# Optimization experiments

Measured on AMD Instinct MI355X. Metric: run time of the kernel, lower is better.

Reference implementation:

```python
import jax, jax.numpy as jnp
import numpy as np

BN_EPS = 1e-5


def conv1d(x, w, b, pad):
    # x: [N, Cin, L], w: [Cout, Cin, K], b: [Cout]
    out = jax.lax.conv_general_dilated(x, w, (1,), [(pad, pad)],
                                       dimension_numbers=("NCH", "OIH", "NCH"))
    return out + b[None, :, None]


def setup_inputs() -> dict:
    key = jax.random.key(0)
    ks = jax.random.split(key, 20)
    N, C, T, V = 64, 64, 256, 25
    S = 3                      # num_subset
    inter = C // 4             # inter_channels = out_channels // coff_embedding
    Cout = C
    ker_jpt = V if V % 2 else V - 1   # 25 -> spatial-attention kernel
    rr = 2

    x = jax.random.normal(ks[0], (N, C, T, V), dtype=jnp.float32)

    PA = 0.1 * jax.random.normal(ks[1], (S, V, V), dtype=jnp.float32)
    alpha = jnp.array([0.1], dtype=jnp.float32)
    Wa = 0.1 * jax.random.normal(ks[2], (S, inter, C), dtype=jnp.float32)
    ba = 0.01 * jax.random.normal(ks[3], (S, inter), dtype=jnp.float32)
    Wb = 0.1 * jax.random.normal(ks[4], (S, inter, C), dtype=jnp.float32)
    bb = 0.01 * jax.random.normal(ks[5], (S, inter), dtype=jnp.float32)
    Wd = 0.1 * jax.random.normal(ks[6], (S, Cout, C), dtype=jnp.float32)
    bd = 0.01 * jax.random.normal(ks[7], (S, Cout), dtype=jnp.float32)

    bn_gamma = 1.0 + 0.1 * jax.random.normal(ks[8], (Cout,), dtype=jnp.float32)
    bn_beta = 0.1 * jax.random.normal(ks[9], (Cout,), dtype=jnp.float32)

    Wsa = 0.05 * jax.random.normal(ks[10], (1, Cout, ker_jpt), dtype=jnp.float32)
    bsa = jnp.zeros((1,), dtype=jnp.float32)
    Wta = 0.05 * jax.random.normal(ks[11], (1, Cout, 9), dtype=jnp.float32)
    bta = jnp.zeros((1,), dtype=jnp.float32)

    W1 = 0.1 * jax.random.normal(ks[12], (Cout // rr, Cout), dtype=jnp.float32)
    b1 = jnp.zeros((Cout // rr,), dtype=jnp.float32)
    W2 = 0.1 * jax.random.normal(ks[13], (Cout, Cout // rr), dtype=jnp.float32)
    b2 = jnp.zeros((Cout,), dtype=jnp.float32)

    return dict(x=x, PA=PA, alpha=alpha, Wa=Wa, ba=ba, Wb=Wb, bb=bb, Wd=Wd, bd=bd,
                bn_gamma=bn_gamma, bn_beta=bn_beta, Wsa=Wsa, bsa=bsa, Wta=Wta,
                bta=bta, W1=W1, b1=b1, W2=W2, b2=b2)


def reference(x, PA, alpha, Wa, ba, Wb, bb, Wd, bd, bn_gamma, bn_beta,
              Wsa, bsa, Wta, bta, W1, b1, W2, b2):
    N, C, T, V = x.shape
    S, inter = Wa.shape[0], Wa.shape[1]
    denom = jnp.float32(inter * T)   # A1.size(-1) after view(N, V, inter*T)

    y = jnp.zeros((N, Wd.shape[1], T, V), dtype=x.dtype)
    for i in range(S):
        # 1x1 convs -> embeddings [N, inter, T, V]
        a = jnp.einsum("nctv,ic->nitv", x, Wa[i]) + ba[i][None, :, None, None]
        bf = jnp.einsum("nctv,ic->nitv", x, Wb[i]) + bb[i][None, :, None, None]
        # adaptive adjacency [N, V, V]
        A1 = jnp.tanh(jnp.einsum("nitv,nitw->nvw", a, bf) / denom)
        Ai = PA[i] + A1 * alpha[0]
        # graph aggregation + 1x1 conv_d
        z = jnp.einsum("nctv,nvw->nctw", x, Ai)
        y = y + jnp.einsum("nctv,oc->notv", z, Wd[i]) + bd[i][None, :, None, None]

    # eval-mode BatchNorm2d (running_mean=0, running_var=1)
    scale = bn_gamma / jnp.sqrt(1.0 + BN_EPS)
    y = y * scale[None, :, None, None] + bn_beta[None, :, None, None]
    # residual (in_channels == out_channels -> identity down)
    y = jax.nn.relu(y + x)

    # spatial SE gate: mean over T -> Conv1d over V
    se = y.mean(axis=2)                                   # [N, C, V]
    g = jax.nn.sigmoid(conv1d(se, Wsa, bsa, (Wsa.shape[-1] - 1) // 2))  # [N,1,V]
    y = y * g[:, :, None, :] + y

    # temporal SE gate: mean over V -> Conv1d over T
    se = y.mean(axis=3)                                   # [N, C, T]
    g = jax.nn.sigmoid(conv1d(se, Wta, bta, 4))           # [N, 1, T]
    y = y * g[:, :, :, None] + y

    # channel SE gate: global mean -> MLP
    se = y.mean(axis=(2, 3))                              # [N, C]
    h = jax.nn.relu(se @ W1.T + b1)
    g = jax.nn.sigmoid(h @ W2.T + b2)                     # [N, C]
    y = y * g[:, :, None, None] + y
    return y
```

## Files before the change

kernel.cpp:

```cpp
#include <hip/hip_runtime.h>
#include <math.h>


typedef __attribute__((ext_vector_type(8))) __bf16 bf16x8;
typedef __attribute__((ext_vector_type(4))) float  f32x4;

#define AIF_HALF 196608

__global__ __launch_bounds__(256, 3) void gcn_kA(const float* __restrict__ x,
                                                 const float* __restrict__ Wa,
                                                 const float* __restrict__ ba,
                                                 const float* __restrict__ Wb,
                                                 const float* __restrict__ bb,
                                                 float* __restrict__ Pws) {
    const int bid = blockIdx.x;
    const int n  = bid >> 4;
    const int tt = bid & 15;
    const int tid  = threadIdx.x;
    const int lane = tid & 63;
    const int wv   = tid >> 6;
    const int col  = lane & 15;
    const int quad = lane >> 4;

    __shared__ __align__(16) __bf16 xB[112 * 72];
    __shared__ __align__(16) __bf16 aT[3][32 * 72];
    __shared__ __align__(16) __bf16 bT[3][32 * 72];

    for (int j = tid; j < 12 * 72; j += 256) xB[100 * 72 + j] = (__bf16)0.f;
    for (int j = tid; j < 7 * 72; j += 256) {
        #pragma unroll
        for (int s = 0; s < 3; ++s) {
            aT[s][25 * 72 + j] = (__bf16)0.f;
            bT[s][25 * 72 + j] = (__bf16)0.f;
        }
    }

    bf16x8 waf0[3], waf1[3], wbf0[3], wbf1[3];
    float ba4[3][4], bb4[3][4];
    #pragma unroll
    for (int s = 0; s < 3; ++s) {
        const float* wap = Wa + (size_t)s * 1024 + col * 64 + quad * 8;
        const float* wbp = Wb + (size_t)s * 1024 + col * 64 + quad * 8;
        #pragma unroll
        for (int j = 0; j < 8; ++j) { waf0[s][j] = (__bf16)wap[j];      wbf0[s][j] = (__bf16)wbp[j]; }
        #pragma unroll
        for (int j = 0; j < 8; ++j) { waf1[s][j] = (__bf16)wap[32 + j]; wbf1[s][j] = (__bf16)wbp[32 + j]; }
        #pragma unroll
        for (int r = 0; r < 4; ++r) {
            ba4[s][r] = ba[s * 16 + quad * 4 + r];
            bb4[s][r] = bb[s * 16 + quad * 4 + r];
        }
    }

    f32x4 pacc[3];
    #pragma unroll
    for (int s = 0; s < 3; ++s) pacc[s] = (f32x4){0.f, 0.f, 0.f, 0.f};
    const int mi = wv >> 1, ni = wv & 1;

    const float* xbase = x + (size_t)n * 409600 + tt * 400;

    for (int cc = 0; cc < 4; ++cc) {
        __syncthreads();
        const float* xc = xbase + cc * 100;
        #pragma unroll
        for (int it = 0; it < 7; ++it) {
            int j4 = tid + it * 256;
            if (j4 < 1600) {
                int c  = j4 / 25;
                int qq = (j4 - c * 25) * 4;
                float4 xv = *(const float4*)(xc + c * 6400 + qq);
                __bf16* dst = &xB[qq * 72 + c];
                dst[0]   = (__bf16)xv.x;
                dst[72]  = (__bf16)xv.y;
                dst[144] = (__bf16)xv.z;
                dst[216] = (__bf16)xv.w;
            }
        }
        __syncthreads();

        #pragma unroll
        for (int s = 0; s < 3; ++s) {
            for (int jt = wv; jt < 7; jt += 4) {
                int q = jt * 16 + col;
                const __bf16* bp = &xB[q * 72 + quad * 8];
                bf16x8 b0 = *(const bf16x8*)bp;
                bf16x8 b1 = *(const bf16x8*)(bp + 32);
                f32x4 da = {0.f, 0.f, 0.f, 0.f}, db = {0.f, 0.f, 0.f, 0.f};
                da = __builtin_amdgcn_mfma_f32_16x16x32_bf16(waf0[s], b0, da, 0, 0, 0);
                da = __builtin_amdgcn_mfma_f32_16x16x32_bf16(waf1[s], b1, da, 0, 0, 0);
                db = __builtin_amdgcn_mfma_f32_16x16x32_bf16(wbf0[s], b0, db, 0, 0, 0);
                db = __builtin_amdgcn_mfma_f32_16x16x32_bf16(wbf1[s], b1, db, 0, 0, 0);
                if (q < 100) {
                    int tl = q / 25, v = q - tl * 25;
                    #pragma unroll
                    for (int r = 0; r < 4; ++r) {
                        int k = (quad * 4 + r) * 4 + tl;
                        aT[s][v * 72 + k] = (__bf16)(da[r] + ba4[s][r]);
                        bT[s][v * 72 + k] = (__bf16)(db[r] + bb4[s][r]);
                    }
                }
            }
        }
        __syncthreads();

        #pragma unroll
        for (int s = 0; s < 3; ++s) {
            #pragma unroll
            for (int k0 = 0; k0 < 64; k0 += 32) {
                bf16x8 af  = *(const bf16x8*)&aT[s][(mi * 16 + col) * 72 + k0 + quad * 8];
                bf16x8 bfr = *(const bf16x8*)&bT[s][(ni * 16 + col) * 72 + k0 + quad * 8];
                pacc[s] = __builtin_amdgcn_mfma_f32_16x16x32_bf16(af, bfr, pacc[s], 0, 0, 0);
            }
        }
    }

    #pragma unroll
    for (int s = 0; s < 3; ++s) {
        #pragma unroll
        for (int r = 0; r < 4; ++r) {
            int v = mi * 16 + quad * 4 + r;
            int w = ni * 16 + col;
            if (v < 25 && w < 25)
                atomicAdd(&Pws[(size_t)(s * 64 + n) * 625 + v * 25 + w], pacc[s][r]);
        }
    }
}

__global__ __launch_bounds__(256) void gcn_kB(const float* __restrict__ Pws,
                                              const float* __restrict__ PA,
                                              const float* __restrict__ alpha,
                                              __bf16* __restrict__ aiF) {
    int j = blockIdx.x * 256 + threadIdx.x;
    if (j < 120000) {
        int sn = j / 625;
        int r  = j - sn * 625;
        int s  = sn >> 6;
        float val = PA[s * 625 + r] + alpha[0] * tanhf(Pws[j] * (1.f / 4096.f));
        int k  = r / 25;
        int nn = r - k * 25;
        int vt = nn >> 4, colx = nn & 15;
        int idx = ((sn * 2 + vt) << 9) + (colx << 5) + k;
        __bf16 h = (__bf16)val;
        aiF[idx]            = h;
        aiF[AIF_HALF + idx] = (__bf16)(val - (float)h);
    }
}

__global__ __launch_bounds__(256, 3) void gcn_kC(const float* __restrict__ x,
                                              const __bf16* __restrict__ aiF,
                                              const float* __restrict__ Wd,
                                              const float* __restrict__ bd,
                                              const float* __restrict__ gamma,
                                              const float* __restrict__ beta,
                                              float* __restrict__ y1,
                                              float* __restrict__ meanT) {
    const int bid = blockIdx.x;
    const int tt = bid & 15;
    const int n  = bid >> 4;
    const int tid  = threadIdx.x;
    const int lane = tid & 63;
    const int wv   = tid >> 6;
    const int col  = lane & 15;
    const int quad = lane >> 4;

    __shared__ __align__(16) __bf16 xB[112 * 72];
    __shared__ __align__(16) __bf16 uL[256 * 40];

    for (int j = tid; j < 12 * 72; j += 256) xB[100 * 72 + j] = (__bf16)0.f;
    for (int j = tid; j < 256 * 15; j += 256) {
        int r = j / 15;
        int e = j - r * 15;
        uL[r * 40 + 25 + e] = (__bf16)0.f;
    }

    bf16x8 aiH[3][2], aiL[3][2];
    #pragma unroll
    for (int s = 0; s < 3; ++s) {
        #pragma unroll
        for (int vt = 0; vt < 2; ++vt) {
            const __bf16* p = aiF + ((size_t)((s * 64 + n) * 2 + vt)) * 512
                                  + col * 32 + quad * 8;
            aiH[s][vt] = *(const bf16x8*)p;
            aiL[s][vt] = *(const bf16x8*)(p + AIF_HALF);
        }
    }

    bf16x8 wd0[3], wd1[3];
    #pragma unroll
    for (int s = 0; s < 3; ++s) {
        const float* wdp = Wd + (size_t)(s * 64 + wv * 16 + col) * 64 + quad * 8;
        #pragma unroll
        for (int j = 0; j < 8; ++j) wd0[s][j] = (__bf16)wdp[j];
        #pragma unroll
        for (int j = 0; j < 8; ++j) wd1[s][j] = (__bf16)wdp[32 + j];
    }

    float scv[4], btv[4], bdsv[4];
    #pragma unroll
    for (int ml = 0; ml < 4; ++ml) {
        int o = (wv * 4 + ml) * 4 + quad;
        scv[ml]  = gamma[o] * rsqrtf(1.f + 1e-5f);
        btv[ml]  = beta[o];
        bdsv[ml] = bd[o] + bd[64 + o] + bd[128 + o];
    }

    float msum[4][2];
    #pragma unroll
    for (int ml = 0; ml < 4; ++ml) { msum[ml][0] = 0.f; msum[ml][1] = 0.f; }

    const float* xbase = x + (size_t)n * 409600 + tt * 400;

    for (int cc = 0; cc < 4; ++cc) {
        f32x4 acc[4][2];
        #pragma unroll
        for (int ml = 0; ml < 4; ++ml) {
            acc[ml][0] = (f32x4){0.f, 0.f, 0.f, 0.f};
            acc[ml][1] = (f32x4){0.f, 0.f, 0.f, 0.f};
        }

        __syncthreads();
        const float* xc = xbase + cc * 100;
        #pragma unroll
        for (int it = 0; it < 7; ++it) {
            int j4 = tid + it * 256;
            if (j4 < 1600) {
                int c  = j4 / 25;
                int qq = (j4 - c * 25) * 4;
                float4 xv = *(const float4*)(xc + c * 6400 + qq);
                __bf16* dst = &xB[qq * 72 + c];
                dst[0]   = (__bf16)xv.x;
                dst[72]  = (__bf16)xv.y;
                dst[144] = (__bf16)xv.z;
                dst[216] = (__bf16)xv.w;
            }
        }
        __syncthreads();

        #pragma unroll
        for (int s = 0; s < 3; ++s) {
            #pragma unroll
            for (int qt = 0; qt < 7; ++qt) {
                const __bf16* bp = &xB[(qt * 16 + col) * 72 + quad * 8];
                bf16x8 b0 = *(const bf16x8*)bp;
                bf16x8 b1 = *(const bf16x8*)(bp + 32);
                f32x4 u = {0.f, 0.f, 0.f, 0.f};
                u = __builtin_amdgcn_mfma_f32_16x16x32_bf16(wd0[s], b0, u, 0, 0, 0);
                u = __builtin_amdgcn_mfma_f32_16x16x32_bf16(wd1[s], b1, u, 0, 0, 0);
                int q = qt * 16 + col;
                if (q < 100) {
                    int trel = q / 25, v = q - trel * 25;
                    int rowbase = ((wv * 16 + quad * 4) * 4 + trel) * 40 + v;
                    uL[rowbase]       = (__bf16)u[0];
                    uL[rowbase + 160] = (__bf16)u[1];
                    uL[rowbase + 320] = (__bf16)u[2];
                    uL[rowbase + 480] = (__bf16)u[3];
                }
            }
            #pragma unroll
            for (int ml = 0; ml < 4; ++ml) {
                int row = (wv * 4 + ml) * 16 + col;
                bf16x8 af = *(const bf16x8*)&uL[row * 40 + quad * 8];
                acc[ml][0] = __builtin_amdgcn_mfma_f32_16x16x32_bf16(af, aiH[s][0], acc[ml][0], 0, 0, 0);
                acc[ml][1] = __builtin_amdgcn_mfma_f32_16x16x32_bf16(af, aiH[s][1], acc[ml][1], 0, 0, 0);
                acc[ml][0] = __builtin_amdgcn_mfma_f32_16x16x32_bf16(af, aiL[s][0], acc[ml][0], 0, 0, 0);
                acc[ml][1] = __builtin_amdgcn_mfma_f32_16x16x32_bf16(af, aiL[s][1], acc[ml][1], 0, 0, 0);
            }
        }

        #pragma unroll
        for (int ml = 0; ml < 4; ++ml) {
            int o = (wv * 4 + ml) * 4 + quad;
            #pragma unroll
            for (int vt = 0; vt < 2; ++vt) {
                int v = vt * 16 + col;
                if (v < 25) {
                    const size_t base =
                        ((size_t)(n * 64 + o) * 256 + tt * 16 + cc * 4) * 25 + v;
                    float ms = 0.f;
                    #pragma unroll
                    for (int r = 0; r < 4; ++r) {
                        float val = scv[ml] * (acc[ml][vt][r] + bdsv[ml]) + btv[ml]
                                  + x[base + r * 25];
                        val = val > 0.f ? val : 0.f;
                        y1[base + r * 25] = val;
                        ms += val;
                    }
                    msum[ml][vt] += ms;
                }
            }
        }
    }

    #pragma unroll
    for (int ml = 0; ml < 4; ++ml) {
        int o = (wv * 4 + ml) * 4 + quad;
        #pragma unroll
        for (int vt = 0; vt < 2; ++vt) {
            int v = vt * 16 + col;
            if (v < 25)
                atomicAdd(&meanT[(n * 64 + o) * 25 + v], msum[ml][vt]);
        }
    }
}

__global__ __launch_bounds__(256) void gcn_kD(const float* __restrict__ meanT,
                                              const float* __restrict__ Wsa,
                                              const float* __restrict__ bsa,
                                              float* __restrict__ g2p) {
    const int n = blockIdx.x;
    const int tid = threadIdx.x;
    __shared__ float sm[1600], wl[1600];
    for (int j = tid; j < 1600; j += 256) {
        sm[j] = meanT[n * 1600 + j] * (1.f / 256.f);
        wl[j] = Wsa[j];
    }
    __syncthreads();
    if (tid < 25) {
        float acc = bsa[0];
        for (int c = 0; c < 64; ++c) {
            #pragma unroll
            for (int k = 0; k < 25; ++k) {
                int j = tid + k - 12;
                if (j >= 0 && j < 25) acc += sm[c * 25 + j] * wl[c * 25 + k];
            }
        }
        g2p[n * 25 + tid] = 1.f + 1.f / (1.f + expf(-acc));
    }
}

__global__ __launch_bounds__(256) void gcn_kE(const float* __restrict__ y1,
                                              const float* __restrict__ g2p,
                                              float* __restrict__ M2) {
    const int bid = blockIdx.x;
    const int n = bid >> 6;
    const int tid = threadIdx.x;
    __shared__ float yl[6400];
    __shared__ float g2l[25];
    const float4* yp = (const float4*)(y1 + (size_t)bid * 6400);
    float4* ylv = (float4*)yl;
    for (int j = tid; j < 1600; j += 256) ylv[j] = yp[j];
    if (tid < 25) g2l[tid] = g2p[n * 25 + tid];
    __syncthreads();
    float sum = 0.f;
    #pragma unroll
    for (int v = 0; v < 25; ++v) sum += yl[tid * 25 + v] * g2l[v];
    M2[bid * 256 + tid] = sum * 0.04f;
}

__global__ __launch_bounds__(256) void gcn_kFG(const float* __restrict__ M2,
                                               const float* __restrict__ Wta,
                                               const float* __restrict__ bta,
                                               const float* __restrict__ W1,
                                               const float* __restrict__ b1,
                                               const float* __restrict__ W2,
                                               const float* __restrict__ b2,
                                               float* __restrict__ g3p,
                                               float* __restrict__ g4p) {
    const int n = blockIdx.x;
    const int tid = threadIdx.x;
    __shared__ float m2L[64 * 260];
    __shared__ float wl[576];
    __shared__ float g3l[256], part[256], M3[64], h[32];

    for (int j = tid; j < 16384; j += 256) {
        int c = j >> 8, t = j & 255;
        m2L[c * 260 + t] = M2[(size_t)n * 16384 + j];
    }
    for (int j = tid; j < 576; j += 256) wl[j] = Wta[j];
    __syncthreads();

    {
        const int t = tid;
        float acc = bta[0];
        for (int c = 0; c < 64; ++c) {
            const float* mp = &m2L[c * 260];
            #pragma unroll
            for (int k = 0; k < 9; ++k) {
                int j = t + k - 4;
                if (j >= 0 && j < 256) acc += mp[j] * wl[c * 9 + k];
            }
        }
        float g3 = 1.f + 1.f / (1.f + expf(-acc));
        g3l[t] = g3;
        g3p[n * 256 + t] = g3;
    }
    __syncthreads();

    {
        const int c = tid >> 2, q = tid & 3;
        float p = 0.f;
        const float* mp = &m2L[c * 260 + q * 64];
        #pragma unroll 16
        for (int j = 0; j < 64; ++j) p += mp[j] * g3l[q * 64 + j];
        part[tid] = p;
    }
    __syncthreads();
    if (tid < 64)
        M3[tid] = (part[tid * 4] + part[tid * 4 + 1] + part[tid * 4 + 2] +
                   part[tid * 4 + 3]) * (1.f / 256.f);
    __syncthreads();
    if (tid < 32) {
        float acc = b1[tid];
        #pragma unroll 16
        for (int cc = 0; cc < 64; ++cc) acc += W1[tid * 64 + cc] * M3[cc];
        h[tid] = acc > 0.f ? acc : 0.f;
    }
    __syncthreads();
    if (tid < 64) {
        float acc = b2[tid];
        #pragma unroll
        for (int j = 0; j < 32; ++j) acc += W2[tid * 32 + j] * h[j];
        g4p[n * 64 + tid] = 1.f + 1.f / (1.f + expf(-acc));
    }
}

__global__ __launch_bounds__(256) void gcn_kH(float* __restrict__ y,
                                              const float* __restrict__ g2p,
                                              const float* __restrict__ g3p,
                                              const float* __restrict__ g4p) {
    const int bid = blockIdx.x;
    const int n = bid >> 6;
    const int tid = threadIdx.x;
    __shared__ float g3l[256], g2l[25];
    g3l[tid] = g3p[n * 256 + tid];
    if (tid < 25) g2l[tid] = g2p[n * 25 + tid];
    const float g4 = g4p[bid];
    __syncthreads();
    float4* yp = (float4*)(y + (size_t)bid * 6400);
    for (int f = tid; f < 1600; f += 256) {
        float4 val = yp[f];
        float* vv = (float*)&val;
        const int base = f * 4;
        #pragma unroll
        for (int k = 0; k < 4; ++k) {
            int idx = base + k;
            int t = (int)(((unsigned long long)idx * 1374389535ull) >> 35);
            int v = idx - t * 25;
            vv[k] *= g2l[v] * g3l[t] * g4;
        }
        yp[f] = val;
    }
}

extern "C" void kernel_launch(void* const* d_in, const int* in_sizes, int n_in,
                              void* d_out, int out_size, void* d_ws, size_t ws_size,
                              hipStream_t stream) {
    const float* x     = (const float*)d_in[0];
    const float* PA    = (const float*)d_in[1];
    const float* alpha = (const float*)d_in[2];
    const float* Wa    = (const float*)d_in[3];
    const float* ba    = (const float*)d_in[4];
    const float* Wb    = (const float*)d_in[5];
    const float* bb    = (const float*)d_in[6];
    const float* Wd    = (const float*)d_in[7];
    const float* bd    = (const float*)d_in[8];
    const float* gamma = (const float*)d_in[9];
    const float* beta  = (const float*)d_in[10];
    const float* Wsa   = (const float*)d_in[11];
    const float* bsa   = (const float*)d_in[12];
    const float* Wta   = (const float*)d_in[13];
    const float* bta   = (const float*)d_in[14];
    const float* W1    = (const float*)d_in[15];
    const float* b1    = (const float*)d_in[16];
    const float* W2    = (const float*)d_in[17];
    const float* b2    = (const float*)d_in[18];

    float* out = (float*)d_out;
    float* ws  = (float*)d_ws;

    float*  Pws   = ws;
    float*  meanT = ws + 120000;
    __bf16* aiF   = (__bf16*)(ws + 222400);
    float*  M2    = ws + 419008;
    float*  g2p   = ws + 4613312;
    float*  g3p   = ws + 4614912;
    float*  g4p   = ws + 4631296;

    hipMemsetAsync(ws, 0, 222400 * sizeof(float), stream);
    hipMemsetAsync(aiF, 0, 786432, stream);

    gcn_kA<<<1024, 256, 0, stream>>>(x, Wa, ba, Wb, bb, Pws);
    gcn_kB<<<469, 256, 0, stream>>>(Pws, PA, alpha, aiF);
    gcn_kC<<<1024, 256, 0, stream>>>(x, aiF, Wd, bd, gamma, beta, out, meanT);
    gcn_kD<<<64, 256, 0, stream>>>(meanT, Wsa, bsa, g2p);
    gcn_kE<<<4096, 256, 0, stream>>>(out, g2p, M2);
    gcn_kFG<<<64, 256, 0, stream>>>(M2, Wta, bta, W1, b1, W2, b2, g3p, g4p);
    gcn_kH<<<4096, 256, 0, stream>>>(out, g2p, g3p, g4p);
}
```

Baseline: 593.9 us.

## Stage gcn_kC epilogue through per-wave LDS for coalesced float4 output stores

Each wave now owns 16 output channels end to end. It loads x as float4 once and keeps those values in registers for the residual, which removes the second scalar global read of x in the epilogue. The BN-scaled accumulators are first written to a per-wave LDS buffer (aliased with the uL scratch). They are then read back, combined with x, passed through ReLU, and written to y1 as coalesced float4 stores. Partial row sums are reduced through LDS atomics before the global atomicAdd. The cost is more LDS traffic, extra registers for the cached x vectors, and per-wave re-zeroing of the padding.

```diff
diff --git a/kernel.cpp b/kernel.cpp
--- a/kernel.cpp
+++ b/kernel.cpp
@@ -164,13 +164,16 @@
     const int quad = lane >> 4;
 
     __shared__ __align__(16) __bf16 xB[112 * 72];
-    __shared__ __align__(16) __bf16 uL[256 * 40];
+    __shared__ __align__(16) unsigned char uY[4 * 6656];
+
+    __bf16* uLw = (__bf16*)(uY + wv * 6656);
+    float*  ySw = (float*) (uY + wv * 6656);
 
     for (int j = tid; j < 12 * 72; j += 256) xB[100 * 72 + j] = (__bf16)0.f;
-    for (int j = tid; j < 256 * 15; j += 256) {
-        int r = j / 15;
-        int e = j - r * 15;
-        uL[r * 40 + 25 + e] = (__bf16)0.f;
+    {
+        __bf16* rz = uLw + lane * 40;
+        #pragma unroll
+        for (int k = 25; k < 32; ++k) rz[k] = (__bf16)0.f;
     }
 
     bf16x8 aiH[3][2], aiL[3][2];
@@ -198,17 +201,18 @@
     float scv[4], btv[4], bdsv[4];
     #pragma unroll
     for (int ml = 0; ml < 4; ++ml) {
-        int o = (wv * 4 + ml) * 4 + quad;
+        int o = wv * 16 + ml * 4 + quad;
         scv[ml]  = gamma[o] * rsqrtf(1.f + 1e-5f);
         btv[ml]  = beta[o];
         bdsv[ml] = bd[o] + bd[64 + o] + bd[128 + o];
     }
 
-    float msum[4][2];
-    #pragma unroll
-    for (int ml = 0; ml < 4; ++ml) { msum[ml][0] = 0.f; msum[ml][1] = 0.f; }
-
-    const float* xbase = x + (size_t)n * 409600 + tt * 400;
+    f32x4 msA[7];
+    #pragma unroll
+    for (int it = 0; it < 7; ++it) msA[it] = (f32x4){0.f, 0.f, 0.f, 0.f};
+
+    const float* xgw = x  + (size_t)(n * 64 + wv * 16) * 6400 + tt * 400;
+    float*       ygw = y1 + (size_t)(n * 64 + wv * 16) * 6400 + tt * 400;
 
     for (int cc = 0; cc < 4; ++cc) {
         f32x4 acc[4][2];
@@ -219,19 +223,21 @@
         }
 
         __syncthreads();
-        const float* xc = xbase + cc * 100;
+        const float* xc = xgw + cc * 100;
+        float4 xv[7];
         #pragma unroll
         for (int it = 0; it < 7; ++it) {
-            int j4 = tid + it * 256;
-            if (j4 < 1600) {
-                int c  = j4 / 25;
-                int qq = (j4 - c * 25) * 4;
-                float4 xv = *(const float4*)(xc + c * 6400 + qq);
+            int j = lane + it * 64;
+            if (j < 400) {
+                int cl = j / 25;
+                int qq = (j - cl * 25) * 4;
+                xv[it] = *(const float4*)(xc + cl * 6400 + qq);
+                int c = wv * 16 + cl;
                 __bf16* dst = &xB[qq * 72 + c];
-                dst[0]   = (__bf16)xv.x;
-                dst[72]  = (__bf16)xv.y;
-                dst[144] = (__bf16)xv.z;
-                dst[216] = (__bf16)xv.w;
+                dst[0]   = (__bf16)xv[it].x;
+                dst[72]  = (__bf16)xv[it].y;
+                dst[144] = (__bf16)xv[it].z;
+                dst[216] = (__bf16)xv[it].w;
             }
         }
         __syncthreads();
@@ -249,17 +255,16 @@
                 int q = qt * 16 + col;
                 if (q < 100) {
                     int trel = q / 25, v = q - trel * 25;
-                    int rowbase = ((wv * 16 + quad * 4) * 4 + trel) * 40 + v;
-                    uL[rowbase]       = (__bf16)u[0];
-                    uL[rowbase + 160] = (__bf16)u[1];
-                    uL[rowbase + 320] = (__bf16)u[2];
-                    uL[rowbase + 480] = (__bf16)u[3];
+                    int rowbase = (quad * 16 + trel) * 40 + v;
+                    uLw[rowbase]       = (__bf16)u[0];
+                    uLw[rowbase + 160] = (__bf16)u[1];
+                    uLw[rowbase + 320] = (__bf16)u[2];
+                    uLw[rowbase + 480] = (__bf16)u[3];
                 }
             }
             #pragma unroll
             for (int ml = 0; ml < 4; ++ml) {
-                int row = (wv * 4 + ml) * 16 + col;
-                bf16x8 af = *(const bf16x8*)&uL[row * 40 + quad * 8];
+                bf16x8 af = *(const bf16x8*)&uLw[(ml * 16 + col) * 40 + quad * 8];
                 acc[ml][0] = __builtin_amdgcn_mfma_f32_16x16x32_bf16(af, aiH[s][0], acc[ml][0], 0, 0, 0);
                 acc[ml][1] = __builtin_amdgcn_mfma_f32_16x16x32_bf16(af, aiH[s][1], acc[ml][1], 0, 0, 0);
                 acc[ml][0] = __builtin_amdgcn_mfma_f32_16x16x32_bf16(af, aiL[s][0], acc[ml][0], 0, 0, 0);
@@ -269,37 +274,67 @@
 
         #pragma unroll
         for (int ml = 0; ml < 4; ++ml) {
-            int o = (wv * 4 + ml) * 4 + quad;
+            int ol = ml * 4 + quad;
             #pragma unroll
             for (int vt = 0; vt < 2; ++vt) {
                 int v = vt * 16 + col;
                 if (v < 25) {
-                    const size_t base =
-                        ((size_t)(n * 64 + o) * 256 + tt * 16 + cc * 4) * 25 + v;
-                    float ms = 0.f;
                     #pragma unroll
-                    for (int r = 0; r < 4; ++r) {
-                        float val = scv[ml] * (acc[ml][vt][r] + bdsv[ml]) + btv[ml]
-                                  + x[base + r * 25];
-                        val = val > 0.f ? val : 0.f;
-                        y1[base + r * 25] = val;
-                        ms += val;
-                    }
-                    msum[ml][vt] += ms;
+                    for (int r = 0; r < 4; ++r)
+                        ySw[ol * 104 + r * 25 + v] =
+                            scv[ml] * (acc[ml][vt][r] + bdsv[ml]) + btv[ml];
                 }
             }
         }
-    }
-
-    #pragma unroll
-    for (int ml = 0; ml < 4; ++ml) {
-        int o = (wv * 4 + ml) * 4 + quad;
-        #pragma unroll
-        for (int vt = 0; vt < 2; ++vt) {
-            int v = vt * 16 + col;
-            if (v < 25)
-                atomicAdd(&meanT[(n * 64 + o) * 25 + v], msum[ml][vt]);
-        }
+
+        float* yc2 = ygw + cc * 100;
+        #pragma unroll
+        for (int it = 0; it < 7; ++it) {
+            int j = lane + it * 64;
+            if (j < 400) {
+                int cl = j / 25;
+                int qq = (j - cl * 25) * 4;
+                f32x4 yv = *(const f32x4*)&ySw[cl * 104 + qq];
+                float4 o4;
+                o4.x = yv[0] + xv[it].x; o4.x = o4.x > 0.f ? o4.x : 0.f;
+                o4.y = yv[1] + xv[it].y; o4.y = o4.y > 0.f ? o4.y : 0.f;
+                o4.z = yv[2] + xv[it].z; o4.z = o4.z > 0.f ? o4.z : 0.f;
+                o4.w = yv[3] + xv[it].w; o4.w = o4.w > 0.f ? o4.w : 0.f;
+                *(float4*)(yc2 + cl * 6400 + qq) = o4;
+                msA[it][0] += o4.x;
+                msA[it][1] += o4.y;
+                msA[it][2] += o4.z;
+                msA[it][3] += o4.w;
+            }
+        }
+
+        {
+            __bf16* rz = uLw + lane * 40;
+            #pragma unroll
+            for (int k = 25; k < 32; ++k) rz[k] = (__bf16)0.f;
+        }
+    }
+
+    __syncthreads();
+    float* msW = (float*)xB + wv * 1008;
+    for (int j2 = lane; j2 < 400; j2 += 64) msW[j2] = 0.f;
+    #pragma unroll
+    for (int it = 0; it < 7; ++it) {
+        int j = lane + it * 64;
+        if (j < 400) {
+            int cl = j / 25;
+            int qq = (j - cl * 25) * 4;
+            #pragma unroll
+            for (int k = 0; k < 4; ++k) {
+                int q = qq + k;
+                int v = q >= 75 ? q - 75 : (q >= 50 ? q - 50 : (q >= 25 ? q - 25 : q));
+                atomicAdd(&msW[cl * 25 + v], msA[it][k]);
+            }
+        }
+    }
+    for (int j2 = lane; j2 < 400; j2 += 64) {
+        int cl = j2 / 25, v = j2 - cl * 25;
+        atomicAdd(&meanT[(n * 64 + wv * 16 + cl) * 25 + v], msW[j2]);
     }
 }
 
```

After: 671.3 us. +13.0%, slower.

## Stage GCN output through per-wave LDS for coalesced stores and reuse staged residual

Applied to the files above, without the earlier changes.

gcn_kC's intermediate LDS buffer becomes a per-wave region that also serves as a float staging area for the output tile. Results are then written to y1 as coalesced float4 rows instead of scattered scalar stores. The residual is now read from the bf16 copy of x already in LDS rather than re-read from global memory. This cuts global traffic and uncoalesced stores, but the residual is rounded to bf16, and the padding columns must be re-zeroed every chunk because the staging area overlaps them.

```diff
diff --git a/kernel.cpp b/kernel.cpp
--- a/kernel.cpp
+++ b/kernel.cpp
@@ -164,13 +164,16 @@
     const int quad = lane >> 4;
 
     __shared__ __align__(16) __bf16 xB[112 * 72];
-    __shared__ __align__(16) __bf16 uL[256 * 40];
+    __shared__ __align__(16) unsigned char uY[4 * 6656];
+
+    __bf16* uLw = (__bf16*)(uY + wv * 6656);
+    float*  ySw = (float*) (uY + wv * 6656);
 
     for (int j = tid; j < 12 * 72; j += 256) xB[100 * 72 + j] = (__bf16)0.f;
-    for (int j = tid; j < 256 * 15; j += 256) {
-        int r = j / 15;
-        int e = j - r * 15;
-        uL[r * 40 + 25 + e] = (__bf16)0.f;
+    {
+        __bf16* rz = uLw + lane * 40;
+        #pragma unroll
+        for (int k = 25; k < 32; ++k) rz[k] = (__bf16)0.f;
     }
 
     bf16x8 aiH[3][2], aiL[3][2];
@@ -198,7 +201,7 @@
     float scv[4], btv[4], bdsv[4];
     #pragma unroll
     for (int ml = 0; ml < 4; ++ml) {
-        int o = (wv * 4 + ml) * 4 + quad;
+        int o = wv * 16 + ml * 4 + quad;
         scv[ml]  = gamma[o] * rsqrtf(1.f + 1e-5f);
         btv[ml]  = beta[o];
         bdsv[ml] = bd[o] + bd[64 + o] + bd[128 + o];
@@ -209,6 +212,7 @@
     for (int ml = 0; ml < 4; ++ml) { msum[ml][0] = 0.f; msum[ml][1] = 0.f; }
 
     const float* xbase = x + (size_t)n * 409600 + tt * 400;
+    float*       ygw   = y1 + (size_t)(n * 64 + wv * 16) * 6400 + tt * 400;
 
     for (int cc = 0; cc < 4; ++cc) {
         f32x4 acc[4][2];
@@ -249,17 +253,16 @@
                 int q = qt * 16 + col;
                 if (q < 100) {
                     int trel = q / 25, v = q - trel * 25;
-                    int rowbase = ((wv * 16 + quad * 4) * 4 + trel) * 40 + v;
-                    uL[rowbase]       = (__bf16)u[0];
-                    uL[rowbase + 160] = (__bf16)u[1];
-                    uL[rowbase + 320] = (__bf16)u[2];
-                    uL[rowbase + 480] = (__bf16)u[3];
+                    int rowbase = (quad * 16 + trel) * 40 + v;
+                    uLw[rowbase]       = (__bf16)u[0];
+                    uLw[rowbase + 160] = (__bf16)u[1];
+                    uLw[rowbase + 320] = (__bf16)u[2];
+                    uLw[rowbase + 480] = (__bf16)u[3];
                 }
             }
             #pragma unroll
             for (int ml = 0; ml < 4; ++ml) {
-                int row = (wv * 4 + ml) * 16 + col;
-                bf16x8 af = *(const bf16x8*)&uL[row * 40 + quad * 8];
+                bf16x8 af = *(const bf16x8*)&uLw[(ml * 16 + col) * 40 + quad * 8];
                 acc[ml][0] = __builtin_amdgcn_mfma_f32_16x16x32_bf16(af, aiH[s][0], acc[ml][0], 0, 0, 0);
                 acc[ml][1] = __builtin_amdgcn_mfma_f32_16x16x32_bf16(af, aiH[s][1], acc[ml][1], 0, 0, 0);
                 acc[ml][0] = __builtin_amdgcn_mfma_f32_16x16x32_bf16(af, aiL[s][0], acc[ml][0], 0, 0, 0);
@@ -269,31 +272,51 @@
 
         #pragma unroll
         for (int ml = 0; ml < 4; ++ml) {
-            int o = (wv * 4 + ml) * 4 + quad;
+            int ol = ml * 4 + quad;
+            int o  = wv * 16 + ol;
             #pragma unroll
             for (int vt = 0; vt < 2; ++vt) {
                 int v = vt * 16 + col;
                 if (v < 25) {
-                    const size_t base =
-                        ((size_t)(n * 64 + o) * 256 + tt * 16 + cc * 4) * 25 + v;
                     float ms = 0.f;
                     #pragma unroll
                     for (int r = 0; r < 4; ++r) {
+                        float resid = (float)xB[(r * 25 + v) * 72 + o];
                         float val = scv[ml] * (acc[ml][vt][r] + bdsv[ml]) + btv[ml]
-                                  + x[base + r * 25];
+                                  + resid;
                         val = val > 0.f ? val : 0.f;
-                        y1[base + r * 25] = val;
+                        ySw[ol * 104 + r * 25 + v] = val;
                         ms += val;
                     }
                     msum[ml][vt] += ms;
                 }
             }
         }
+
+        float* yc2 = ygw + cc * 100;
+        #pragma unroll
+        for (int it = 0; it < 7; ++it) {
+            int j = lane + it * 64;
+            if (j < 400) {
+                int cl = j / 25;
+                int qq = (j - cl * 25) * 4;
+                f32x4 yv = *(const f32x4*)&ySw[cl * 104 + qq];
+                float4 o4;
+                o4.x = yv[0]; o4.y = yv[1]; o4.z = yv[2]; o4.w = yv[3];
+                *(float4*)(yc2 + cl * 6400 + qq) = o4;
+            }
+        }
+
+        {
+            __bf16* rz = uLw + lane * 40;
+            #pragma unroll
+            for (int k = 25; k < 32; ++k) rz[k] = (__bf16)0.f;
+        }
     }
 
     #pragma unroll
     for (int ml = 0; ml < 4; ++ml) {
-        int o = (wv * 4 + ml) * 4 + quad;
+        int o = wv * 16 + ml * 4 + quad;
         #pragma unroll
         for (int vt = 0; vt < 2; ++vt) {
             int v = vt * 16 + col;
```

Result: slower. 622.5 us (+4.8%).
